# Kernel tuning notes

Measured on AMD Instinct MI355X. Metric: run time of the kernel, lower is better.

Reference implementation:

```python
import math
import jax, jax.numpy as jnp
import numpy as np

BS, Q_LEN, DIM = 8, 16, 4096
MAX_SEQ = 4096
N_Q_HEADS, N_KV_HEADS, HEAD_DIM = 32, 8, 128
REP = N_Q_HEADS // N_KV_HEADS


def setup_inputs() -> dict:
    key = jax.random.key(0)
    ks = jax.random.split(key, 12)
    w = 0.02
    return {
        "x": jax.random.normal(ks[0], (BS, Q_LEN, DIM), jnp.float32),
        "k_cache": jax.random.normal(ks[1], (BS, MAX_SEQ, N_KV_HEADS, HEAD_DIM), jnp.float32),
        "v_cache": jax.random.normal(ks[2], (BS, MAX_SEQ, N_KV_HEADS, HEAD_DIM), jnp.float32),
        "Wq": jax.random.normal(ks[3], (DIM, N_Q_HEADS * HEAD_DIM), jnp.float32) * w,
        "bq": jax.random.normal(ks[4], (N_Q_HEADS * HEAD_DIM,), jnp.float32) * w,
        "Wk": jax.random.normal(ks[5], (DIM, N_KV_HEADS * HEAD_DIM), jnp.float32) * w,
        "bk": jax.random.normal(ks[6], (N_KV_HEADS * HEAD_DIM,), jnp.float32) * w,
        "Wv": jax.random.normal(ks[7], (DIM, N_KV_HEADS * HEAD_DIM), jnp.float32) * w,
        "bv": jax.random.normal(ks[8], (N_KV_HEADS * HEAD_DIM,), jnp.float32) * w,
        "Wo": jax.random.normal(ks[9], (N_Q_HEADS * HEAD_DIM, DIM), jnp.float32) * w,
        "bo": jax.random.normal(ks[10], (DIM,), jnp.float32) * w,
        "start_pos": MAX_SEQ - Q_LEN,
        "seq_len_for_kv": Q_LEN,
    }


def reference(x, k_cache, v_cache, Wq, bq, Wk, bk, Wv, bv, Wo, bo, start_pos, seq_len_for_kv):
    bs, sl, dim = x.shape
    # Projections (torch Linear: x @ W^T + b; here W stored as [in, out])
    q = (x @ Wq + bq).reshape(bs, sl, N_KV_HEADS, REP, HEAD_DIM)  # [b, q, g, r, d]
    k = (x @ Wk + bk).reshape(bs, sl, N_KV_HEADS, HEAD_DIM)
    v = (x @ Wv + bv).reshape(bs, sl, N_KV_HEADS, HEAD_DIM)
    # KV-cache append (start_pos / seq_len_for_kv are static Python ints)
    k_cache = k_cache.at[:, start_pos:start_pos + seq_len_for_kv].set(k)
    v_cache = v_cache.at[:, start_pos:start_pos + seq_len_for_kv].set(v)
    kv_len = start_pos + seq_len_for_kv
    keys = k_cache[:, :kv_len]    # [b, L, g, d]
    vals = v_cache[:, :kv_len]    # [b, L, g, d]
    # GQA: each kv head g serves REP query heads r (broadcast instead of repeat_kv)
    scale = 1.0 / math.sqrt(HEAD_DIM)
    scores = jnp.einsum('bqgrd,blgd->bgrql', q, keys) * scale  # [b, g, r, q, L]
    att = jax.nn.softmax(scores, axis=-1)
    out = jnp.einsum('bgrql,blgd->bqgrd', att, vals)           # [b, q, g, r, d]
    out = out.reshape(bs, sl, N_Q_HEADS * HEAD_DIM)
    return out @ Wo + bo
```

## Files before the change

### kernel.cpp

```cpp
#include <hip/hip_runtime.h>
#include <math.h>

#define DIM       4096
#define NKVH      8
#define HD        128
#define MAX_SEQ   4096
#define START_POS 4080
#define NQKV      6144
#define NCHUNK    8
#define CHUNK     512
#define KS        8
#define ATT_SCALE 0.08838834764831845f

#define WS_PART   0
#define WS_QH     6291456
#define WS_QL     6553600
#define WS_KNEW   6815744
#define WS_VNEW   6946816
#define WS_PM     7077888
#define WS_PL     7110656
#define WS_ATH    7143424
#define WS_ATL    7405568
#define WS_XH     7667712
#define WS_XL     7929856
#define WS_PARTO  WS_PART

typedef __bf16 bf16x8 __attribute__((ext_vector_type(8)));
typedef float  f32x4  __attribute__((ext_vector_type(4)));
typedef unsigned int uintx4 __attribute__((ext_vector_type(4)));

__device__ __forceinline__ unsigned short f2bf(float f) {
    return __builtin_bit_cast(unsigned short, (__bf16)f);
}
__device__ __forceinline__ float bf2f(unsigned short h) {
    union { unsigned int u; float f; } v; v.u = ((unsigned int)h) << 16;
    return v.f;
}
__device__ __forceinline__ void splitbf(float f, unsigned short &h, unsigned short &l) {
    h = f2bf(f);
    l = f2bf(f - bf2f(h));
}
__device__ __forceinline__ bf16x8 ldsfrag(const unsigned short* p) {
    uintx4 u = *(const uintx4*)p;
    return __builtin_bit_cast(bf16x8, u);
}
__device__ __forceinline__ bf16x8 ldsfrag2(const unsigned short* p) {
    union { uint2 u2[2]; bf16x8 v; } u;
    u.u2[0] = *(const uint2*)p;
    u.u2[1] = *(const uint2*)(p + 4);
    return u.v;
}
#define MFMA16(a,b,c) __builtin_amdgcn_mfma_f32_16x16x32_bf16(a, b, c, 0, 0, 0)
#define VCOMP(v,j) ((j)==0?(v).x:((j)==1?(v).y:((j)==2?(v).z:(v).w)))

__global__ __launch_bounds__(256) void split_x_kernel(
    const float* __restrict__ x, unsigned short* __restrict__ xh,
    unsigned short* __restrict__ xl, int n4)
{
    int i = blockIdx.x * 256 + threadIdx.x;
    if (i < n4) {
        float4 v = *(const float4*)(x + (size_t)i * 4);
        ushort4 h, l;
        splitbf(v.x, h.x, l.x);
        splitbf(v.y, h.y, l.y);
        splitbf(v.z, h.z, l.z);
        splitbf(v.w, h.w, l.w);
        *(ushort4*)(xh + (size_t)i * 4) = h;
        *(ushort4*)(xl + (size_t)i * 4) = l;
    }
}

template<int NT>
__device__ __forceinline__ void gemm_body(
    const unsigned short* __restrict__ Ah, const unsigned short* __restrict__ Al,
    const float* __restrict__ W, int ldW, int noff,
    float* __restrict__ part, int partStride, int ncol0, int ks,
    unsigned short* Ahs, unsigned short* Als, unsigned short* Bs)
{
    constexpr int NC4   = NT * 4;
    constexpr int RSTEP = 256 / NC4;
    const int t = threadIdx.x;
    const int w = t >> 6, lane = t & 63, l15 = lane & 15, quad = lane >> 4;
    const int n4 = t & (NC4 - 1);
    const int kk = t / NC4;

    f32x4 acc[2][NT];
    #pragma unroll
    for (int i = 0; i < 2; ++i)
        #pragma unroll
        for (int nt = 0; nt < NT; ++nt) acc[i][nt] = (f32x4){0.f, 0.f, 0.f, 0.f};

    const int k0base = ks * 512;
    float4 wreg[NT];

    auto LOADW = [&](int it) {
        int k0 = k0base + it * 64;
        #pragma unroll
        for (int i = 0; i < NT; ++i)
            wreg[i] = *(const float4*)(W + (size_t)(k0 + kk + RSTEP * i) * ldW + noff + n4 * 4);
    };

    LOADW(0);
    for (int it = 0; it < 8; ++it) {
        int k0 = k0base + it * 64;
        __syncthreads();
        uintx4 ah4[4], al4[4];
        #pragma unroll
        for (int i = 0; i < 4; ++i) {
            int f = t + i * 256;
            int row = f >> 3, c0 = (f & 7) << 3;
            size_t off = (size_t)row * DIM + k0 + c0;
            ah4[i] = *(const uintx4*)(Ah + off);
            al4[i] = *(const uintx4*)(Al + off);
        }
        #pragma unroll
        for (int i = 0; i < NT; ++i)
            #pragma unroll
            for (int j = 0; j < 4; ++j)
                Bs[(n4 * 4 + j) * 68 + kk + RSTEP * i] = f2bf(VCOMP(wreg[i], j));
        #pragma unroll
        for (int i = 0; i < 4; ++i) {
            int f = t + i * 256;
            int row = f >> 3, c0 = (f & 7) << 3;
            *(uintx4*)(Ahs + row * 72 + c0) = ah4[i];
            *(uintx4*)(Als + row * 72 + c0) = al4[i];
        }
        __syncthreads();
        if (it < 7) LOADW(it + 1);
        #pragma unroll
        for (int kt = 0; kt < 2; ++kt) {
            int ko = kt * 32 + quad * 8;
            bf16x8 ah0 = ldsfrag(Ahs + ((2*w+0)*16 + l15) * 72 + ko);
            bf16x8 ah1 = ldsfrag(Ahs + ((2*w+1)*16 + l15) * 72 + ko);
            bf16x8 al0 = ldsfrag(Als + ((2*w+0)*16 + l15) * 72 + ko);
            bf16x8 al1 = ldsfrag(Als + ((2*w+1)*16 + l15) * 72 + ko);
            #pragma unroll
            for (int nt = 0; nt < NT; ++nt) {
                bf16x8 b = ldsfrag2(Bs + (nt*16 + l15) * 68 + ko);
                acc[0][nt] = MFMA16(ah0, b, acc[0][nt]);
                acc[0][nt] = MFMA16(al0, b, acc[0][nt]);
                acc[1][nt] = MFMA16(ah1, b, acc[1][nt]);
                acc[1][nt] = MFMA16(al1, b, acc[1][nt]);
            }
        }
    }
    #pragma unroll
    for (int i = 0; i < 2; ++i)
        #pragma unroll
        for (int nt = 0; nt < NT; ++nt)
            #pragma unroll
            for (int r = 0; r < 4; ++r) {
                int row = (2*w + i) * 16 + quad * 4 + r;
                int col = ncol0 + nt * 16 + l15;
                part[(size_t)(ks * 128 + row) * partStride + col] = acc[i][nt][r];
            }
}

__global__ __launch_bounds__(256, 2) void qkv_gemm_kernel(
    const unsigned short* __restrict__ xh, const unsigned short* __restrict__ xl,
    const float* __restrict__ Wq, const float* __restrict__ Wk,
    const float* __restrict__ Wv, float* __restrict__ part)
{
    __shared__ unsigned short Ahs[128 * 72], Als[128 * 72];
    __shared__ unsigned short Bs[256 * 68];
    int ncol0 = blockIdx.x * 256;
    int ks = blockIdx.y;
    const float* W; int ldW, noff;
    if (ncol0 < 4096)      { W = Wq; ldW = 4096; noff = ncol0; }
    else if (ncol0 < 5120) { W = Wk; ldW = 1024; noff = ncol0 - 4096; }
    else                   { W = Wv; ldW = 1024; noff = ncol0 - 5120; }
    gemm_body<16>(xh, xl, W, ldW, noff, part, NQKV, ncol0, ks, Ahs, Als, Bs);
}

__global__ __launch_bounds__(256, 2) void oproj_gemm_kernel(
    const unsigned short* __restrict__ ah, const unsigned short* __restrict__ al,
    const float* __restrict__ Wo, float* __restrict__ part)
{
    __shared__ unsigned short Ahs[128 * 72], Als[128 * 72];
    __shared__ unsigned short Bs[128 * 68];
    int ncol0 = blockIdx.x * 128;
    int ks = blockIdx.y;
    gemm_body<8>(ah, al, Wo, 4096, ncol0, part, 4096, ncol0, ks, Ahs, Als, Bs);
}

__global__ __launch_bounds__(256) void qkv_reduce_kernel(
    const float* __restrict__ part, const float* __restrict__ bq,
    const float* __restrict__ bk, const float* __restrict__ bv,
    unsigned short* __restrict__ qh, unsigned short* __restrict__ ql,
    float* __restrict__ k_new, float* __restrict__ v_new)
{
    int gid = blockIdx.x * 256 + threadIdx.x;
    int row = gid / 1536;
    int c4  = gid - row * 1536;
    int n = c4 * 4;
    float4 s = make_float4(0.f, 0.f, 0.f, 0.f);
    #pragma unroll
    for (int j = 0; j < KS; ++j) {
        float4 p = *(const float4*)&part[(size_t)(j * 128 + row) * NQKV + n];
        s.x += p.x; s.y += p.y; s.z += p.z; s.w += p.w;
    }
    if (n < 4096) {
        float4 b4 = *(const float4*)&bq[n];
        ushort4 h, l;
        splitbf(s.x + b4.x, h.x, l.x);
        splitbf(s.y + b4.y, h.y, l.y);
        splitbf(s.z + b4.z, h.z, l.z);
        splitbf(s.w + b4.w, h.w, l.w);
        *(ushort4*)&qh[row * 4096 + n] = h;
        *(ushort4*)&ql[row * 4096 + n] = l;
    } else if (n < 5120) {
        float4 b4 = *(const float4*)&bk[n - 4096];
        float4 o = make_float4(s.x + b4.x, s.y + b4.y, s.z + b4.z, s.w + b4.w);
        *(float4*)&k_new[row * 1024 + (n - 4096)] = o;
    } else {
        float4 b4 = *(const float4*)&bv[n - 5120];
        float4 o = make_float4(s.x + b4.x, s.y + b4.y, s.z + b4.z, s.w + b4.w);
        *(float4*)&v_new[row * 1024 + (n - 5120)] = o;
    }
}

__global__ __launch_bounds__(512, 2) void attn_partial6_kernel(
    const unsigned short* __restrict__ qhp, const unsigned short* __restrict__ qlp,
    const float* __restrict__ kc, const float* __restrict__ vc,
    const float* __restrict__ knew, const float* __restrict__ vnew,
    float* __restrict__ part_O, float* __restrict__ part_m, float* __restrict__ part_l)
{
    __shared__ unsigned short Kb[2][32][136];
    __shared__ unsigned short Vt[2][128][44];
    __shared__ unsigned short Pw[8][16 * 36];

    const int t = threadIdx.x;
    const int w = t >> 6, lane = t & 63, l15 = lane & 15, quad = lane >> 4;
    const int gsel = w >> 2;
    const int rep  = w & 3;
    const int blk = blockIdx.x;
    const int b = blk >> 5, gg = (blk >> 3) & 3, c = blk & 7;
    const int g = gg * 2 + gsel;

    const int p0 = t >> 6;
    const int q4 = t & 63;
    const int gl = q4 >> 5;
    const int d0 = (q4 & 31) << 2;

    bf16x8 qhf[4], qlf[4];
    {
        size_t base = (size_t)(b * 16 + l15) * DIM + (g * 4 + rep) * HD + quad * 8;
        #pragma unroll
        for (int kt = 0; kt < 4; ++kt) {
            qhf[kt] = ldsfrag(qhp + base + kt * 32);
            qlf[kt] = ldsfrag(qlp + base + kt * 32);
        }
    }

    float m_run[4], l_run[4];
    f32x4 oacc[8];
    #pragma unroll
    for (int r = 0; r < 4; ++r) { m_run[r] = -INFINITY; l_run[r] = 0.f; }
    #pragma unroll
    for (int d = 0; d < 8; ++d) oacc[d] = (f32x4){0.f, 0.f, 0.f, 0.f};

    float4 kA[4], vA[4], kB[4], vB[4];

    auto LOADKV = [&](float4 (&kr)[4], float4 (&vr)[4], int it) {
        #pragma unroll
        for (int i = 0; i < 4; ++i) {
            int pos = p0 + i * 8;
            int pg = c * CHUNK + it * 32 + pos;
            const float *ksrc, *vsrc;
            if (pg >= START_POS) {
                size_t off = (size_t)(b * 16 + pg - START_POS) * (NKVH * HD) + gg * 256 + q4 * 4;
                ksrc = knew + off; vsrc = vnew + off;
            } else {
                size_t off = ((size_t)(b * MAX_SEQ + pg) * NKVH) * HD + gg * 256 + q4 * 4;
                ksrc = kc + off; vsrc = vc + off;
            }
            kr[i] = *(const float4*)ksrc;
            vr[i] = *(const float4*)vsrc;
        }
    };

    auto STAGE = [&](const float4 (&kr)[4], const float4 (&vr)[4]) {
        #pragma unroll
        for (int i = 0; i < 4; ++i) {
            int pos = p0 + i * 8;
            ushort4 k4 = make_ushort4(f2bf(kr[i].x), f2bf(kr[i].y),
                                      f2bf(kr[i].z), f2bf(kr[i].w));
            *(ushort4*)&Kb[gl][pos][d0] = k4;
        }
        #pragma unroll
        for (int j = 0; j < 4; ++j) {
            ushort4 v4 = make_ushort4(f2bf(VCOMP(vr[0], j)), f2bf(VCOMP(vr[1], j)),
                                      f2bf(VCOMP(vr[2], j)), f2bf(VCOMP(vr[3], j)));
            *(ushort4*)&Vt[gl][d0 + j][p0 * 4] = v4;
        }
    };

    unsigned short* phw = Pw[w];

    auto COMPUTE = [&]() {
        f32x4 sacc[2];
        sacc[0] = (f32x4){0.f,0.f,0.f,0.f};
        sacc[1] = (f32x4){0.f,0.f,0.f,0.f};
        #pragma unroll
        for (int nt = 0; nt < 2; ++nt)
            #pragma unroll
            for (int kt = 0; kt < 4; ++kt) {
                bf16x8 bh = ldsfrag(&Kb[gsel][nt*16 + l15][kt*32 + quad*8]);
                sacc[nt] = MFMA16(qhf[kt], bh, sacc[nt]);
                sacc[nt] = MFMA16(qlf[kt], bh, sacc[nt]);
            }

        float e0[4], e1[4], alpha[4];
        #pragma unroll
        for (int r = 0; r < 4; ++r) {
            float s0 = sacc[0][r] * ATT_SCALE;
            float s1 = sacc[1][r] * ATT_SCALE;
            float mx = fmaxf(s0, s1);
            mx = fmaxf(mx, __shfl_xor(mx, 1));
            mx = fmaxf(mx, __shfl_xor(mx, 2));
            mx = fmaxf(mx, __shfl_xor(mx, 4));
            mx = fmaxf(mx, __shfl_xor(mx, 8));
            float mnew = fmaxf(m_run[r], mx);
            alpha[r] = __expf(m_run[r] - mnew);
            e0[r] = __expf(s0 - mnew);
            e1[r] = __expf(s1 - mnew);
            float sum = e0[r] + e1[r];
            sum += __shfl_xor(sum, 1);
            sum += __shfl_xor(sum, 2);
            sum += __shfl_xor(sum, 4);
            sum += __shfl_xor(sum, 8);
            l_run[r] = l_run[r] * alpha[r] + sum;
            m_run[r] = mnew;
        }
        #pragma unroll
        for (int d = 0; d < 8; ++d)
            #pragma unroll
            for (int r = 0; r < 4; ++r) oacc[d][r] *= alpha[r];

        {
            int slot0 = 4 * (l15 & 7) + (l15 >> 3);
            #pragma unroll
            for (int r = 0; r < 4; ++r) {
                phw[(quad*4 + r) * 36 + slot0]     = f2bf(e0[r]);
                phw[(quad*4 + r) * 36 + slot0 + 2] = f2bf(e1[r]);
            }
        }
        bf16x8 pa = ldsfrag(phw + l15 * 36 + quad * 8);

        #pragma unroll
        for (int dt = 0; dt < 8; ++dt) {
            bf16x8 vb = ldsfrag(&Vt[gsel][dt*16 + l15][quad * 8]);
            oacc[dt] = MFMA16(pa, vb, oacc[dt]);
        }
    };

    LOADKV(kA, vA, 0);
    LOADKV(kB, vB, 1);
    for (int ii = 0; ii < 8; ++ii) {
        __syncthreads();
        STAGE(kA, vA);
        __syncthreads();
        if (ii < 7) LOADKV(kA, vA, 2*ii + 2);
        COMPUTE();
        __syncthreads();
        STAGE(kB, vB);
        __syncthreads();
        if (ii < 7) LOADKV(kB, vB, 2*ii + 3);
        COMPUTE();
    }

    const size_t obase = (size_t)((b * 8 + g) * 8 + c) * 64 + rep * 16 + quad * 4;
    #pragma unroll
    for (int dt = 0; dt < 8; ++dt)
        #pragma unroll
        for (int r = 0; r < 4; ++r)
            part_O[(obase + r) * HD + dt * 16 + l15] = oacc[dt][r];
    if (l15 == 0) {
        #pragma unroll
        for (int r = 0; r < 4; ++r) {
            part_m[obase + r] = m_run[r];
            part_l[obase + r] = l_run[r];
        }
    }
}

__global__ __launch_bounds__(128) void attn_combine_kernel(
    const float* __restrict__ part_O, const float* __restrict__ part_m,
    const float* __restrict__ part_l, unsigned short* __restrict__ ah,
    unsigned short* __restrict__ al)
{
    int bid = blockIdx.x;
    int d = threadIdx.x;
    int bg = bid >> 6;
    int row = bid & 63;
    float mc[NCHUNK], lc[NCHUNK];
    float M = -INFINITY;
    #pragma unroll
    for (int cc = 0; cc < NCHUNK; ++cc) {
        mc[cc] = part_m[(bg * NCHUNK + cc) * 64 + row];
        lc[cc] = part_l[(bg * NCHUNK + cc) * 64 + row];
        M = fmaxf(M, mc[cc]);
    }
    float L = 0.f, acc = 0.f;
    #pragma unroll
    for (int cc = 0; cc < NCHUNK; ++cc) {
        float wgt = __expf(mc[cc] - M);
        L += lc[cc] * wgt;
        acc += part_O[((size_t)(bg * NCHUNK + cc) * 64 + row) * HD + d] * wgt;
    }
    int b = bg >> 3, g = bg & 7;
    int r = row >> 4, qp = row & 15;
    float v = acc / L;
    unsigned short h, l; splitbf(v, h, l);
    size_t idx = (size_t)(b * 16 + qp) * DIM + (g * 4 + r) * HD + d;
    ah[idx] = h; al[idx] = l;
}

__global__ __launch_bounds__(256) void oproj_reduce_kernel(
    const float* __restrict__ part, const float* __restrict__ bo,
    float* __restrict__ out)
{
    int gid4 = blockIdx.x * 256 + threadIdx.x;
    int n = (gid4 & 1023) * 4;
    float4 s = make_float4(0.f, 0.f, 0.f, 0.f);
    #pragma unroll
    for (int j = 0; j < KS; ++j) {
        float4 p = *(const float4*)&part[(size_t)j * 524288 + (size_t)gid4 * 4];
        s.x += p.x; s.y += p.y; s.z += p.z; s.w += p.w;
    }
    float4 b4 = *(const float4*)&bo[n];
    float4 o = make_float4(s.x + b4.x, s.y + b4.y, s.z + b4.z, s.w + b4.w);
    *(float4*)&out[(size_t)gid4 * 4] = o;
}

extern "C" void kernel_launch(void* const* d_in, const int* in_sizes, int n_in,
                              void* d_out, int out_size, void* d_ws, size_t ws_size,
                              hipStream_t stream)
{
    const float* x  = (const float*)d_in[0];
    const float* kc = (const float*)d_in[1];
    const float* vc = (const float*)d_in[2];
    const float* Wq = (const float*)d_in[3];
    const float* bq = (const float*)d_in[4];
    const float* Wk = (const float*)d_in[5];
    const float* bk = (const float*)d_in[6];
    const float* Wv = (const float*)d_in[7];
    const float* bv = (const float*)d_in[8];
    const float* Wo = (const float*)d_in[9];
    const float* bo = (const float*)d_in[10];
    float* out = (float*)d_out;
    float* ws  = (float*)d_ws;

    unsigned short* xh = (unsigned short*)(ws + WS_XH);
    unsigned short* xl = (unsigned short*)(ws + WS_XL);
    unsigned short* qh = (unsigned short*)(ws + WS_QH);
    unsigned short* ql = (unsigned short*)(ws + WS_QL);
    unsigned short* ath = (unsigned short*)(ws + WS_ATH);
    unsigned short* atl = (unsigned short*)(ws + WS_ATL);

    split_x_kernel<<<512, 256, 0, stream>>>(x, xh, xl, 131072);
    qkv_gemm_kernel<<<dim3(24, KS), 256, 0, stream>>>(xh, xl, Wq, Wk, Wv, ws + WS_PART);
    qkv_reduce_kernel<<<768, 256, 0, stream>>>(ws + WS_PART, bq, bk, bv,
                                               qh, ql, ws + WS_KNEW, ws + WS_VNEW);
    attn_partial6_kernel<<<256, 512, 0, stream>>>(qh, ql, kc, vc,
                                                  ws + WS_KNEW, ws + WS_VNEW,
                                                  ws + WS_PARTO, ws + WS_PM, ws + WS_PL);
    attn_combine_kernel<<<4096, 128, 0, stream>>>(ws + WS_PARTO, ws + WS_PM,
                                                  ws + WS_PL, ath, atl);
    oproj_gemm_kernel<<<dim3(32, KS), 256, 0, stream>>>(ath, atl, Wo, ws + WS_PART);
    oproj_reduce_kernel<<<512, 256, 0, stream>>>(ws + WS_PART, bo, out);
}
```

Measured before the change: 457.8 us.

## Shrink QKV GEMM tiles, prefetch A with W, coalesce epilogue, single-buffer attention

The QKV GEMM moves from 256-column tiles to 128-column tiles, doubling the grid to 48x8 blocks. Both GEMMs now prefetch the A fragments for the next k-step together with W, and use one shared-memory arena. The GEMM epilogue stages accumulators through LDS so each row of partials is written with coalesced float4 stores instead of scattered scalar stores. The attention kernel drops its two-register-set double-buffered KV prefetch for a single prefetch set, which cuts register pressure but gives less latency hiding.

```diff
diff --git a/kernel.cpp b/kernel.cpp
--- a/kernel.cpp
+++ b/kernel.cpp
@@ -75,14 +75,17 @@
     const unsigned short* __restrict__ Ah, const unsigned short* __restrict__ Al,
     const float* __restrict__ W, int ldW, int noff,
     float* __restrict__ part, int partStride, int ncol0, int ks,
-    unsigned short* Ahs, unsigned short* Als, unsigned short* Bs)
-{
+    unsigned short* smem)
+{
+    unsigned short* Ahs = smem;
+    unsigned short* Als = smem + 9216;
+    unsigned short* Bs  = smem + 18432;
     constexpr int NC4   = NT * 4;
     constexpr int RSTEP = 256 / NC4;
     const int t = threadIdx.x;
     const int w = t >> 6, lane = t & 63, l15 = lane & 15, quad = lane >> 4;
-    const int n4 = t & (NC4 - 1);
-    const int kk = t / NC4;
+    const int n4  = t & (NC4 - 1);
+    const int kkw = t / NC4;
 
     f32x4 acc[2][NT];
     #pragma unroll
@@ -91,42 +94,41 @@
         for (int nt = 0; nt < NT; ++nt) acc[i][nt] = (f32x4){0.f, 0.f, 0.f, 0.f};
 
     const int k0base = ks * 512;
+    uintx4 areg_h[4], areg_l[4];
     float4 wreg[NT];
 
-    auto LOADW = [&](int it) {
+    auto LOAD = [&](int it) {
         int k0 = k0base + it * 64;
-        #pragma unroll
-        for (int i = 0; i < NT; ++i)
-            wreg[i] = *(const float4*)(W + (size_t)(k0 + kk + RSTEP * i) * ldW + noff + n4 * 4);
-    };
-
-    LOADW(0);
-    for (int it = 0; it < 8; ++it) {
-        int k0 = k0base + it * 64;
-        __syncthreads();
-        uintx4 ah4[4], al4[4];
         #pragma unroll
         for (int i = 0; i < 4; ++i) {
             int f = t + i * 256;
             int row = f >> 3, c0 = (f & 7) << 3;
             size_t off = (size_t)row * DIM + k0 + c0;
-            ah4[i] = *(const uintx4*)(Ah + off);
-            al4[i] = *(const uintx4*)(Al + off);
+            areg_h[i] = *(const uintx4*)(Ah + off);
+            areg_l[i] = *(const uintx4*)(Al + off);
         }
         #pragma unroll
         for (int i = 0; i < NT; ++i)
-            #pragma unroll
-            for (int j = 0; j < 4; ++j)
-                Bs[(n4 * 4 + j) * 68 + kk + RSTEP * i] = f2bf(VCOMP(wreg[i], j));
+            wreg[i] = *(const float4*)(W + (size_t)(k0 + kkw + RSTEP * i) * ldW + noff + n4 * 4);
+    };
+
+    LOAD(0);
+    for (int it = 0; it < 8; ++it) {
+        __syncthreads();
         #pragma unroll
         for (int i = 0; i < 4; ++i) {
             int f = t + i * 256;
             int row = f >> 3, c0 = (f & 7) << 3;
-            *(uintx4*)(Ahs + row * 72 + c0) = ah4[i];
-            *(uintx4*)(Als + row * 72 + c0) = al4[i];
-        }
-        __syncthreads();
-        if (it < 7) LOADW(it + 1);
+            *(uintx4*)(Ahs + row * 72 + c0) = areg_h[i];
+            *(uintx4*)(Als + row * 72 + c0) = areg_l[i];
+        }
+        #pragma unroll
+        for (int i = 0; i < NT; ++i)
+            #pragma unroll
+            for (int j = 0; j < 4; ++j)
+                Bs[(n4 * 4 + j) * 68 + kkw + RSTEP * i] = f2bf(VCOMP(wreg[i], j));
+        __syncthreads();
+        if (it < 7) LOAD(it + 1);
         #pragma unroll
         for (int kt = 0; kt < 2; ++kt) {
             int ko = kt * 32 + quad * 8;
@@ -144,16 +146,29 @@
             }
         }
     }
-    #pragma unroll
-    for (int i = 0; i < 2; ++i)
+
+    constexpr int BN   = NT * 16;
+    constexpr int EROW = BN + 4;
+    float* eps = (float*)smem;
+    #pragma unroll
+    for (int i = 0; i < 2; ++i) {
+        __syncthreads();
         #pragma unroll
         for (int nt = 0; nt < NT; ++nt)
             #pragma unroll
-            for (int r = 0; r < 4; ++r) {
-                int row = (2*w + i) * 16 + quad * 4 + r;
-                int col = ncol0 + nt * 16 + l15;
-                part[(size_t)(ks * 128 + row) * partStride + col] = acc[i][nt][r];
-            }
+            for (int r = 0; r < 4; ++r)
+                eps[(w*16 + quad*4 + r) * EROW + nt*16 + l15] = acc[i][nt][r];
+        __syncthreads();
+        #pragma unroll
+        for (int s = 0; s < (64 * NC4) / 256; ++s) {
+            int idx  = t + s * 256;
+            int lrow = idx / NC4;
+            int c4   = idx & (NC4 - 1);
+            int grow = (2 * (lrow >> 4) + i) * 16 + (lrow & 15);
+            f32x4 v = *(const f32x4*)&eps[lrow * EROW + c4 * 4];
+            *(f32x4*)&part[(size_t)(ks * 128 + grow) * partStride + ncol0 + c4 * 4] = v;
+        }
+    }
 }
 
 __global__ __launch_bounds__(256, 2) void qkv_gemm_kernel(
@@ -161,26 +176,24 @@
     const float* __restrict__ Wq, const float* __restrict__ Wk,
     const float* __restrict__ Wv, float* __restrict__ part)
 {
-    __shared__ unsigned short Ahs[128 * 72], Als[128 * 72];
-    __shared__ unsigned short Bs[256 * 68];
-    int ncol0 = blockIdx.x * 256;
+    __shared__ __align__(16) unsigned short smem[27136];
+    int ncol0 = blockIdx.x * 128;
     int ks = blockIdx.y;
     const float* W; int ldW, noff;
     if (ncol0 < 4096)      { W = Wq; ldW = 4096; noff = ncol0; }
     else if (ncol0 < 5120) { W = Wk; ldW = 1024; noff = ncol0 - 4096; }
     else                   { W = Wv; ldW = 1024; noff = ncol0 - 5120; }
-    gemm_body<16>(xh, xl, W, ldW, noff, part, NQKV, ncol0, ks, Ahs, Als, Bs);
+    gemm_body<8>(xh, xl, W, ldW, noff, part, NQKV, ncol0, ks, smem);
 }
 
 __global__ __launch_bounds__(256, 2) void oproj_gemm_kernel(
     const unsigned short* __restrict__ ah, const unsigned short* __restrict__ al,
     const float* __restrict__ Wo, float* __restrict__ part)
 {
-    __shared__ unsigned short Ahs[128 * 72], Als[128 * 72];
-    __shared__ unsigned short Bs[128 * 68];
+    __shared__ __align__(16) unsigned short smem[27136];
     int ncol0 = blockIdx.x * 128;
     int ks = blockIdx.y;
-    gemm_body<8>(ah, al, Wo, 4096, ncol0, part, 4096, ncol0, ks, Ahs, Als, Bs);
+    gemm_body<8>(ah, al, Wo, 4096, ncol0, part, 4096, ncol0, ks, smem);
 }
 
 __global__ __launch_bounds__(256) void qkv_reduce_kernel(
@@ -219,7 +232,7 @@
     }
 }
 
-__global__ __launch_bounds__(512, 2) void attn_partial6_kernel(
+__global__ __launch_bounds__(512, 2) void attn_partial5_kernel(
     const unsigned short* __restrict__ qhp, const unsigned short* __restrict__ qlp,
     const float* __restrict__ kc, const float* __restrict__ vc,
     const float* __restrict__ knew, const float* __restrict__ vnew,
@@ -259,9 +272,8 @@
     #pragma unroll
     for (int d = 0; d < 8; ++d) oacc[d] = (f32x4){0.f, 0.f, 0.f, 0.f};
 
-    float4 kA[4], vA[4], kB[4], vB[4];
-
-    auto LOADKV = [&](float4 (&kr)[4], float4 (&vr)[4], int it) {
+    float4 kreg[4], vreg[4];
+    auto LOADKV = [&](int it) {
         #pragma unroll
         for (int i = 0; i < 4; ++i) {
             int pos = p0 + i * 8;
@@ -274,30 +286,32 @@
                 size_t off = ((size_t)(b * MAX_SEQ + pg) * NKVH) * HD + gg * 256 + q4 * 4;
                 ksrc = kc + off; vsrc = vc + off;
             }
-            kr[i] = *(const float4*)ksrc;
-            vr[i] = *(const float4*)vsrc;
+            kreg[i] = *(const float4*)ksrc;
+            vreg[i] = *(const float4*)vsrc;
         }
     };
 
-    auto STAGE = [&](const float4 (&kr)[4], const float4 (&vr)[4]) {
+    unsigned short* phw = Pw[w];
+
+    LOADKV(0);
+    for (int it = 0; it < 16; ++it) {
+        __syncthreads();
         #pragma unroll
         for (int i = 0; i < 4; ++i) {
             int pos = p0 + i * 8;
-            ushort4 k4 = make_ushort4(f2bf(kr[i].x), f2bf(kr[i].y),
-                                      f2bf(kr[i].z), f2bf(kr[i].w));
+            ushort4 k4 = make_ushort4(f2bf(kreg[i].x), f2bf(kreg[i].y),
+                                      f2bf(kreg[i].z), f2bf(kreg[i].w));
             *(ushort4*)&Kb[gl][pos][d0] = k4;
         }
         #pragma unroll
         for (int j = 0; j < 4; ++j) {
-            ushort4 v4 = make_ushort4(f2bf(VCOMP(vr[0], j)), f2bf(VCOMP(vr[1], j)),
-                                      f2bf(VCOMP(vr[2], j)), f2bf(VCOMP(vr[3], j)));
+            ushort4 v4 = make_ushort4(f2bf(VCOMP(vreg[0], j)), f2bf(VCOMP(vreg[1], j)),
+                                      f2bf(VCOMP(vreg[2], j)), f2bf(VCOMP(vreg[3], j)));
             *(ushort4*)&Vt[gl][d0 + j][p0 * 4] = v4;
         }
-    };
-
-    unsigned short* phw = Pw[w];
-
-    auto COMPUTE = [&]() {
+        __syncthreads();
+        if (it + 1 < 16) LOADKV(it + 1);
+
         f32x4 sacc[2];
         sacc[0] = (f32x4){0.f,0.f,0.f,0.f};
         sacc[1] = (f32x4){0.f,0.f,0.f,0.f};
@@ -352,21 +366,6 @@
             bf16x8 vb = ldsfrag(&Vt[gsel][dt*16 + l15][quad * 8]);
             oacc[dt] = MFMA16(pa, vb, oacc[dt]);
         }
-    };
-
-    LOADKV(kA, vA, 0);
-    LOADKV(kB, vB, 1);
-    for (int ii = 0; ii < 8; ++ii) {
-        __syncthreads();
-        STAGE(kA, vA);
-        __syncthreads();
-        if (ii < 7) LOADKV(kA, vA, 2*ii + 2);
-        COMPUTE();
-        __syncthreads();
-        STAGE(kB, vB);
-        __syncthreads();
-        if (ii < 7) LOADKV(kB, vB, 2*ii + 3);
-        COMPUTE();
     }
 
     const size_t obase = (size_t)((b * 8 + g) * 8 + c) * 64 + rep * 16 + quad * 4;
@@ -459,10 +458,10 @@
     unsigned short* atl = (unsigned short*)(ws + WS_ATL);
 
     split_x_kernel<<<512, 256, 0, stream>>>(x, xh, xl, 131072);
-    qkv_gemm_kernel<<<dim3(24, KS), 256, 0, stream>>>(xh, xl, Wq, Wk, Wv, ws + WS_PART);
+    qkv_gemm_kernel<<<dim3(48, KS), 256, 0, stream>>>(xh, xl, Wq, Wk, Wv, ws + WS_PART);
     qkv_reduce_kernel<<<768, 256, 0, stream>>>(ws + WS_PART, bq, bk, bv,
                                                qh, ql, ws + WS_KNEW, ws + WS_VNEW);
-    attn_partial6_kernel<<<256, 512, 0, stream>>>(qh, ql, kc, vc,
+    attn_partial5_kernel<<<256, 512, 0, stream>>>(qh, ql, kc, vc,
                                                   ws + WS_KNEW, ws + WS_VNEW,
                                                   ws + WS_PARTO, ws + WS_PM, ws + WS_PL);
     attn_combine_kernel<<<4096, 128, 0, stream>>>(ws + WS_PARTO, ws + WS_PM,
```

Result: faster. 440.0 us (-3.9%).
